# Performance work log

Measured on AMD Instinct MI355X. Metric: run time of the kernel, lower is better.

## Reference

```python
import jax, jax.numpy as jnp
import numpy as np

N_NODES = 20000
N_EDGES = 320000
IN_DIM = 256
OUT_DIM = 256
NUM_RELS = 8
NUM_BASES = 4


def setup_inputs() -> dict:
    key = jax.random.key(0)
    k = jax.random.split(key, 7)
    return {
        "h": jax.random.normal(k[0], (N_NODES, IN_DIM), dtype=jnp.float32),
        "basis": jax.random.normal(k[1], (NUM_BASES, IN_DIM, OUT_DIM), dtype=jnp.float32)
        * (6.0 / (IN_DIM + OUT_DIM)) ** 0.5,
        "w_comp": jax.random.normal(k[2], (NUM_RELS, NUM_BASES), dtype=jnp.float32),
        "bias": jax.random.normal(k[3], (OUT_DIM,), dtype=jnp.float32) * 0.01,
        "src": jax.random.randint(k[4], (N_EDGES,), 0, N_NODES, dtype=jnp.int32),
        "dst": jax.random.randint(k[5], (N_EDGES,), 0, N_NODES, dtype=jnp.int32),
        "etype": jax.random.randint(k[6], (N_EDGES,), 0, NUM_RELS, dtype=jnp.int32),
    }


def reference(h, basis, w_comp, bias, src, dst, etype):
    # Faithful to the torch basis-decomposition quirk:
    #   weight.view(in, B, out); matmul(w_comp, .) -> [in, R, out]; view -> [R, in, out]
    in_dim, out_dim = h.shape[1], basis.shape[2]
    num_rels = w_comp.shape[0]
    wr = basis.reshape(in_dim, NUM_BASES, out_dim)          # raw-buffer reinterpret (torch .view)
    weight = jnp.einsum("rb,ibo->iro", w_comp, wr)          # [in, R, out]
    weight = weight.reshape(num_rels, in_dim, out_dim)      # raw-buffer reinterpret (torch .view)

    # msg_e = h[src_e] @ weight[etype_e]. Group by relation: transform all nodes
    # under every relation weight (dense GEMMs), then gather per edge.
    t = jnp.einsum("nd,rdo->rno", h, weight)                # [R, N, out]
    msg = t[etype, src]                                     # [E, out]

    # scatter-sum aggregation to destination nodes (dgl fn.sum)
    agg = jax.ops.segment_sum(msg, dst, num_segments=h.shape[0])  # [N, out]
    return jax.nn.relu(agg + bias)
```

## Files before the change

### kernel.cpp

```cpp
#include <hip/hip_runtime.h>


#define N_NODES  20000
#define N_EDGES  320000
#define IN_DIM   256
#define OUT_DIM  256
#define NUM_RELS 8
#define KDIM     128
#define M_PAD    20032
#define SUBCAP   16

#define FOLD_BLOCKS 2500
#define FILL_BLOCKS 1250
#define BP_BLOCKS   128

typedef __attribute__((ext_vector_type(8)))  short short8;
typedef __attribute__((ext_vector_type(16))) float float16v;

static __device__ __forceinline__ unsigned f2bf_rne(float x) {
    unsigned u = __float_as_uint(x);
    return (u + 0x7fffu + ((u >> 16) & 1u)) >> 16;
}

__global__ __launch_bounds__(256)
void prep_kernel(const float* __restrict__ h, const float* __restrict__ w_comp,
                 unsigned short* __restrict__ U,
                 const int* __restrict__ src, const int* __restrict__ dst,
                 const int* __restrict__ et,
                 int* __restrict__ cnt2, unsigned short* __restrict__ bucket2,
                 const float* __restrict__ basis, unsigned short* __restrict__ Bp) {
    int b = blockIdx.x;
    int t = threadIdx.x;
    if (b < FOLD_BLOCKS) {
        int gid = b * 256 + t;
        int n = gid >> 5, k = gid & 31;
        const float* hp = h + (size_t)n * IN_DIM + k * 8;
        float4 h0 = *(const float4*)hp;
        float4 h1 = *(const float4*)(hp + 4);
        float hv[8] = {h0.x, h0.y, h0.z, h0.w, h1.x, h1.y, h1.z, h1.w};
        float a0 = 0.f, a1 = 0.f, a2 = 0.f, a3 = 0.f;
#pragma unroll
        for (int j = 0; j < 8; ++j) {
            float hj = hv[j];
            a0 += hj * w_comp[j * 4 + 0];
            a1 += hj * w_comp[j * 4 + 1];
            a2 += hj * w_comp[j * 4 + 2];
            a3 += hj * w_comp[j * 4 + 3];
        }
        uint2 p;
        p.x = f2bf_rne(a0) | (f2bf_rne(a1) << 16);
        p.y = f2bf_rne(a2) | (f2bf_rne(a3) << 16);
        *(uint2*)(U + ((size_t)n << 7) + k * 4) = p;
    } else if (b < FOLD_BLOCKS + FILL_BLOCKS) {
        int e = (b - FOLD_BLOCKS) * 256 + t;
        int g = dst[e] * 8 + et[e];
        int p = atomicAdd(&cnt2[g], 1);
        if (p < SUBCAP) bucket2[(g << 4) + p] = (unsigned short)src[e];
    } else {
        int frag = (b - FOLD_BLOCKS - FILL_BLOCKS) * 256 + t;
        int lane = frag & 63;
        int ks   = (frag >> 6) & 7;
        int r    = (frag >> 9) & 7;
        int ct   = frag >> 12;
        int o  = ct * 32 + (lane & 31);
        int kb = r * 128 + ks * 16 + (lane >> 5) * 8;
        const float* bsp = basis + (size_t)kb * 256 + o;
        unsigned v[8];
#pragma unroll
        for (int j = 0; j < 8; ++j) v[j] = f2bf_rne(bsp[(size_t)j * 256]);
        uint4 p;
        p.x = v[0] | (v[1] << 16);
        p.y = v[2] | (v[3] << 16);
        p.z = v[4] | (v[5] << 16);
        p.w = v[6] | (v[7] << 16);
        *(uint4*)(Bp + (size_t)frag * 8) = p;
    }
}

__global__ __launch_bounds__(256)
void aggregate_kernel(const unsigned short* __restrict__ U,
                      const int* __restrict__ cnt2,
                      const unsigned short* __restrict__ bucket2,
                      unsigned int* __restrict__ S) {
    int wid  = threadIdx.x >> 6;
    int lane = threadIdx.x & 63;
    int half = lane >> 5;
    int l32  = lane & 31;
    int d = blockIdx.x * 4 + wid;

    float4 acc[NUM_RELS];
#pragma unroll
    for (int r = 0; r < NUM_RELS; ++r) acc[r] = make_float4(0.f, 0.f, 0.f, 0.f);

    if (d < N_NODES) {
        int base = d * 8;
        int4 ca = *(const int4*)(cnt2 + base);
        int4 cb = *(const int4*)(cnt2 + base + 4);
        int c[8] = {ca.x, ca.y, ca.z, ca.w, cb.x, cb.y, cb.z, cb.w};
#pragma unroll
        for (int r = 0; r < 8; ++r) if (c[r] > SUBCAP) c[r] = SUBCAP;

        uint2 ga[8];
#pragma unroll
        for (int r = 0; r < 8; ++r) {
            int s = bucket2[((base + r) << 4) + half];
            ga[r] = *(const uint2*)(U + ((size_t)s << 7) + l32 * 4);
        }
#pragma unroll
        for (int r = 0; r < 8; ++r) {
            if (half < c[r]) {
                acc[r].x += __uint_as_float(ga[r].x << 16);
                acc[r].y += __uint_as_float(ga[r].x & 0xffff0000u);
                acc[r].z += __uint_as_float(ga[r].y << 16);
                acc[r].w += __uint_as_float(ga[r].y & 0xffff0000u);
            }
        }
#pragma unroll
        for (int r = 0; r < 8; ++r) {
            for (int i = 2; i < c[r]; i += 2) {
                int s = bucket2[((base + r) << 4) + i + half];
                uint2 g = *(const uint2*)(U + ((size_t)s << 7) + l32 * 4);
                if (i + half < c[r]) {
                    acc[r].x += __uint_as_float(g.x << 16);
                    acc[r].y += __uint_as_float(g.x & 0xffff0000u);
                    acc[r].z += __uint_as_float(g.y << 16);
                    acc[r].w += __uint_as_float(g.y & 0xffff0000u);
                }
            }
        }
    }
#pragma unroll
    for (int r = 0; r < NUM_RELS; ++r) {
        acc[r].x += __shfl_xor(acc[r].x, 32);
        acc[r].y += __shfl_xor(acc[r].y, 32);
        acc[r].z += __shfl_xor(acc[r].z, 32);
        acc[r].w += __shfl_xor(acc[r].w, 32);
    }
    if (half == 0) {
#pragma unroll
        for (int r = 0; r < NUM_RELS; ++r) {
            uint2 p;
            p.x = f2bf_rne(acc[r].x) | (f2bf_rne(acc[r].y) << 16);
            p.y = f2bf_rne(acc[r].z) | (f2bf_rne(acc[r].w) << 16);
            *(uint2*)(S + (((size_t)r * M_PAD + d) << 6) + l32 * 2) = p;
        }
    }
}

__global__ __launch_bounds__(512)
void gemm_kernel(const unsigned short* __restrict__ S,
                 const unsigned short* __restrict__ Bp,
                 const float* __restrict__ bias,
                 float* __restrict__ out) {
    __shared__ unsigned short At[64][136];
    int t = threadIdx.x;
    int w = t >> 6, lane = t & 63;
    int ln = lane & 31, hi = lane >> 5;
    int n0 = blockIdx.x * 64;
    int c0 = w * 32;

    int srow = t >> 3, sq = t & 7;
    const unsigned short* sbase = S + (((size_t)n0 + srow) << 7) + sq * 16;
    uint4 pre0 = *(const uint4*)sbase;
    uint4 pre1 = *(const uint4*)(sbase + 8);

    float16v acc0 = {};
    float16v acc1 = {};

    for (int r = 0; r < NUM_RELS; ++r) {
        if (r > 0) __syncthreads();
        *(uint4*)&At[srow][sq * 16] = pre0;
        *(uint4*)&At[srow][sq * 16 + 8] = pre1;
        __syncthreads();
        if (r + 1 < NUM_RELS) {
            const unsigned short* nb = sbase + (((size_t)(r + 1) * M_PAD) << 7);
            pre0 = *(const uint4*)nb;
            pre1 = *(const uint4*)(nb + 8);
        }
        const unsigned short* bpr = Bp + (((size_t)(w * 8 + r) * 8) << 9) + lane * 8;
#pragma unroll
        for (int ks = 0; ks < 8; ++ks) {
            short8 bo = *(const short8*)(bpr + (ks << 9));
            short8 a0 = *(const short8*)&At[ln][ks * 16 + hi * 8];
            short8 a1 = *(const short8*)&At[ln + 32][ks * 16 + hi * 8];
            acc0 = __builtin_amdgcn_mfma_f32_32x32x16_bf16(a0, bo, acc0, 0, 0, 0);
            acc1 = __builtin_amdgcn_mfma_f32_32x32x16_bf16(a1, bo, acc1, 0, 0, 0);
        }
    }

    float bs = bias[c0 + ln];
#pragma unroll
    for (int reg = 0; reg < 16; ++reg) {
        int row = (reg & 3) + 8 * (reg >> 2) + 4 * hi;
        int n = n0 + row;
        if (n < N_NODES)
            out[(size_t)n * OUT_DIM + c0 + ln] = fmaxf(acc0[reg] + bs, 0.f);
        int n2 = n0 + 32 + row;
        if (n2 < N_NODES)
            out[(size_t)n2 * OUT_DIM + c0 + ln] = fmaxf(acc1[reg] + bs, 0.f);
    }
}

extern "C" void kernel_launch(void* const* d_in, const int* in_sizes, int n_in,
                              void* d_out, int out_size, void* d_ws, size_t ws_size,
                              hipStream_t stream) {
    const float* h      = (const float*)d_in[0];
    const float* basis  = (const float*)d_in[1];
    const float* w_comp = (const float*)d_in[2];
    const float* bias   = (const float*)d_in[3];
    const int*   src    = (const int*)d_in[4];
    const int*   dst    = (const int*)d_in[5];
    const int*   etype  = (const int*)d_in[6];
    float*       out    = (float*)d_out;

    char* ws = (char*)d_ws;
    size_t off = 0;
    unsigned short* U   = (unsigned short*)(ws + off); off += (size_t)N_NODES * KDIM * 2;
    unsigned int*   S   = (unsigned int*)(ws + off);   off += (size_t)NUM_RELS * M_PAD * KDIM * 2;
    unsigned short* Bp  = (unsigned short*)(ws + off); off += (size_t)8 * 8 * 8 * 64 * 8 * 2;
    int* cnt2 = (int*)(ws + off); off += (size_t)M_PAD * 8 * 4;
    unsigned short* bucket2 = (unsigned short*)(ws + off);
    off += ((size_t)M_PAD * 8 * SUBCAP + 128) * 2;

    hipMemsetAsync(cnt2, 0, (size_t)N_NODES * 8 * 4, stream);

    prep_kernel<<<FOLD_BLOCKS + FILL_BLOCKS + BP_BLOCKS, 256, 0, stream>>>(
        h, w_comp, U, src, dst, etype, cnt2, bucket2, basis, Bp);

    aggregate_kernel<<<M_PAD / 4, 256, 0, stream>>>(U, cnt2, bucket2, S);

    gemm_kernel<<<M_PAD / 64, 512, 0, stream>>>((const unsigned short*)S, Bp, bias, out);
}
```

Baseline: 153.8 us.

## Write aggregated features in MFMA fragment layout and drop LDS staging in GEMM

The aggregate kernel now stores its bf16 per-relation sums directly in the MFMA A-fragment order, grouped by 32-row tiles. The GEMM can then load each fragment straight from global memory with one short8 per lane, with no LDS tile and no __syncthreads. The GEMM is also reshaped into 256-thread blocks that each cover half of the 256 output columns over a 64-row panel, with one flat 64-step K loop. The launch grid of M_PAD/16 blocks gives twice the 64-row panels actually needed. The extra blocks read past the valid S region and compute results that are never stored, because their rows fail the node-bound check.

After: 166.4 us. +8.2%, slower.

```diff
diff --git a/kernel.cpp b/kernel.cpp
--- a/kernel.cpp
+++ b/kernel.cpp
@@ -137,55 +137,48 @@
         acc[r].w += __shfl_xor(acc[r].w, 32);
     }
     if (half == 0) {
+        int g   = d >> 5;
+        int ks  = l32 >> 2;
+        int hi2 = (l32 >> 1) & 1;
+        int flane = (d & 31) + (hi2 << 5);
+        size_t u0 = ((((size_t)g << 3) << 3) + ks) << 8;
+        int addl = (flane << 2) + ((l32 & 1) << 1);
 #pragma unroll
         for (int r = 0; r < NUM_RELS; ++r) {
             uint2 p;
             p.x = f2bf_rne(acc[r].x) | (f2bf_rne(acc[r].y) << 16);
             p.y = f2bf_rne(acc[r].z) | (f2bf_rne(acc[r].w) << 16);
-            *(uint2*)(S + (((size_t)r * M_PAD + d) << 6) + l32 * 2) = p;
-        }
-    }
-}
-
-__global__ __launch_bounds__(512)
-void gemm_kernel(const unsigned short* __restrict__ S,
+            *(uint2*)(S + u0 + ((size_t)r << 11) + addl) = p;
+        }
+    }
+}
+
+__global__ __launch_bounds__(256)
+void gemm_kernel(const unsigned short* __restrict__ Sf,
                  const unsigned short* __restrict__ Bp,
                  const float* __restrict__ bias,
                  float* __restrict__ out) {
-    __shared__ unsigned short At[64][136];
     int t = threadIdx.x;
     int w = t >> 6, lane = t & 63;
     int ln = lane & 31, hi = lane >> 5;
-    int n0 = blockIdx.x * 64;
-    int c0 = w * 32;
-
-    int srow = t >> 3, sq = t & 7;
-    const unsigned short* sbase = S + (((size_t)n0 + srow) << 7) + sq * 16;
-    uint4 pre0 = *(const uint4*)sbase;
-    uint4 pre1 = *(const uint4*)(sbase + 8);
+    int rp = blockIdx.x >> 1, ch = blockIdx.x & 1;
+    int ct = (ch << 2) | w;
+    int n0 = rp * 64;
+    int c0 = ct * 32;
+
+    const unsigned short* a0p = Sf + (((size_t)rp << 1) << 15) + lane * 8;
+    const unsigned short* a1p = a0p + 32768;
+    const unsigned short* bp  = Bp + ((size_t)ct << 15) + lane * 8;
 
     float16v acc0 = {};
     float16v acc1 = {};
-
-    for (int r = 0; r < NUM_RELS; ++r) {
-        if (r > 0) __syncthreads();
-        *(uint4*)&At[srow][sq * 16] = pre0;
-        *(uint4*)&At[srow][sq * 16 + 8] = pre1;
-        __syncthreads();
-        if (r + 1 < NUM_RELS) {
-            const unsigned short* nb = sbase + (((size_t)(r + 1) * M_PAD) << 7);
-            pre0 = *(const uint4*)nb;
-            pre1 = *(const uint4*)(nb + 8);
-        }
-        const unsigned short* bpr = Bp + (((size_t)(w * 8 + r) * 8) << 9) + lane * 8;
-#pragma unroll
-        for (int ks = 0; ks < 8; ++ks) {
-            short8 bo = *(const short8*)(bpr + (ks << 9));
-            short8 a0 = *(const short8*)&At[ln][ks * 16 + hi * 8];
-            short8 a1 = *(const short8*)&At[ln + 32][ks * 16 + hi * 8];
-            acc0 = __builtin_amdgcn_mfma_f32_32x32x16_bf16(a0, bo, acc0, 0, 0, 0);
-            acc1 = __builtin_amdgcn_mfma_f32_32x32x16_bf16(a1, bo, acc1, 0, 0, 0);
-        }
+#pragma unroll 8
+    for (int f = 0; f < 64; ++f) {
+        short8 bo = *(const short8*)(bp  + ((size_t)f << 9));
+        short8 a0 = *(const short8*)(a0p + ((size_t)f << 9));
+        short8 a1 = *(const short8*)(a1p + ((size_t)f << 9));
+        acc0 = __builtin_amdgcn_mfma_f32_32x32x16_bf16(a0, bo, acc0, 0, 0, 0);
+        acc1 = __builtin_amdgcn_mfma_f32_32x32x16_bf16(a1, bo, acc1, 0, 0, 0);
     }
 
     float bs = bias[c0 + ln];
@@ -229,5 +222,5 @@
 
     aggregate_kernel<<<M_PAD / 4, 256, 0, stream>>>(U, cnt2, bucket2, S);
 
-    gemm_kernel<<<M_PAD / 64, 512, 0, stream>>>((const unsigned short*)S, Bp, bias, out);
-}
+    gemm_kernel<<<M_PAD / 16, 256, 0, stream>>>((const unsigned short*)S, Bp, bias, out);
+}
```
